# Kernel tuning notes

Measured on AMD Instinct MI355X. Metric: run time of the kernel, lower is better.

The kernel has to match this reference:

```python
import jax, jax.numpy as jnp
import numpy as np

HEADS = 4
DIM_HEAD = 64
DIM = 256
FMAP = 64
SCALE = DIM_HEAD ** -0.5


def setup_inputs() -> dict:
    key = jax.random.key(0)
    k1, k2, k3, k4 = jax.random.split(key, 4)
    inner = HEADS * DIM_HEAD
    fmap = jax.random.normal(k1, (4, DIM, FMAP, FMAP), dtype=jnp.float32)
    # 1x1 conv weight for qkv projection: (3*inner_dim, dim)
    w_qkv = jax.random.normal(k2, (3 * inner, DIM), dtype=jnp.float32) * (DIM ** -0.5)
    # AbsPosEmb parameters, initialized as randn * dim_head**-0.5 (as in BoTNet)
    pos_height = jax.random.normal(k3, (FMAP, DIM_HEAD), dtype=jnp.float32) * SCALE
    pos_width = jax.random.normal(k4, (FMAP, DIM_HEAD), dtype=jnp.float32) * SCALE
    return {"fmap": fmap, "w_qkv": w_qkv, "pos_height": pos_height, "pos_width": pos_width}


def reference(fmap, w_qkv, pos_height, pos_width):
    b, c, h, w = fmap.shape
    hw = h * w
    # 1x1 conv (no bias) == channel matmul
    qkv = jnp.einsum('bchw,oc->bohw', fmap, w_qkv)  # (b, 3*inner, h, w)
    q, k, v = jnp.split(qkv, 3, axis=1)
    # replicate torch .view(b, heads, h*w, -1): raw row-major reshape
    q = q.reshape(b, HEADS, hw, DIM_HEAD) * SCALE
    k = k.reshape(b, HEADS, hw, DIM_HEAD)
    v = v.reshape(b, HEADS, hw, DIM_HEAD)
    sim = jnp.einsum('bhid,bhjd->bhij', q, k)  # (b, heads, hw, hw)
    # absolute positional bias: emb[j] = height[y] + width[x], j = y*w + x
    emb = (pos_height[:, None, :] + pos_width[None, :, :]).reshape(hw, DIM_HEAD)
    sim = sim + jnp.einsum('bhid,jd->bhij', q, emb)
    attn = jax.nn.softmax(sim, axis=-1)
    out = jnp.einsum('bhij,bhjd->bhid', attn, v)  # (b, heads, hw, dim_head)
    # replicate torch .view(b, heads*dim_head, h, w): raw reshape
    return out.reshape(b, HEADS * DIM_HEAD, h, w)
```

## Files before the change

### kernel.cpp

```cpp
#include <hip/hip_runtime.h>


typedef float  f32x4  __attribute__((ext_vector_type(4)));
typedef __bf16 bf16x8 __attribute__((ext_vector_type(8)));
typedef __bf16 bf16x4 __attribute__((ext_vector_type(4)));

__device__ inline float fast_exp2(float x) {
#if __has_builtin(__builtin_amdgcn_exp2f)
  return __builtin_amdgcn_exp2f(x);
#else
  return exp2f(x);
#endif
}

__global__ __launch_bounds__(256) void qkv_proj(
    const float* __restrict__ fmap, const float* __restrict__ w,
    const float* __restrict__ ph,   const float* __restrict__ pw,
    __bf16* __restrict__ Qw, __bf16* __restrict__ Kw, __bf16* __restrict__ Vw)
{
  constexpr int LS = 136;
  __shared__ __bf16 As[64 * LS];
  __shared__ __bf16 Bs[64 * LS];
  const int tid  = threadIdx.x;
  const int wv   = tid >> 6;
  const int lane = tid & 63;
  const int quad = lane >> 4, l15 = lane & 15;
  const int n0 = blockIdx.x * 64;
  const int m0 = blockIdx.y * 64;
  const int b  = blockIdx.z;

  f32x4 sacc[4] = {};

  for (int ks = 0; ks < 2; ++ks) {
    const int kbase = ks * 128;
#pragma unroll
    for (int i = 0; i < 8; ++i) {
      int id = tid + i * 256;
      int r  = id >> 5;
      int c4 = (id & 31) * 4;
      f32x4 v = *(const f32x4*)(w + (size_t)(m0 + r) * 256 + kbase + c4);
      bf16x4 o; o[0]=(__bf16)v[0]; o[1]=(__bf16)v[1]; o[2]=(__bf16)v[2]; o[3]=(__bf16)v[3];
      *(bf16x4*)(&As[r * LS + c4]) = o;
    }
#pragma unroll
    for (int i = 0; i < 2; ++i) {
      int id = tid + i * 256;
      int sg = id & 15;
      int kg = id >> 4;
      const float* base = fmap + ((size_t)b * 256 + kbase + 4 * kg) * 4096 + n0 + 4 * sg;
      f32x4 v0 = *(const f32x4*)(base);
      f32x4 v1 = *(const f32x4*)(base + 4096);
      f32x4 v2 = *(const f32x4*)(base + 8192);
      f32x4 v3 = *(const f32x4*)(base + 12288);
#pragma unroll
      for (int j = 0; j < 4; ++j) {
        bf16x4 o; o[0]=(__bf16)v0[j]; o[1]=(__bf16)v1[j]; o[2]=(__bf16)v2[j]; o[3]=(__bf16)v3[j];
        *(bf16x4*)(&Bs[(4 * sg + j) * LS + 4 * kg]) = o;
      }
    }
    __syncthreads();
#pragma unroll
    for (int k0 = 0; k0 < 128; k0 += 32) {
      bf16x8 af = *(const bf16x8*)(&As[(16 * wv + l15) * LS + k0 + 8 * quad]);
#pragma unroll
      for (int t = 0; t < 4; ++t) {
        bf16x8 bt = *(const bf16x8*)(&Bs[(16 * t + l15) * LS + k0 + 8 * quad]);
        sacc[t] = __builtin_amdgcn_mfma_f32_16x16x32_bf16(af, bt, sacc[t], 0, 0, 0);
      }
    }
    __syncthreads();
  }

  const int region = blockIdx.y >> 2;
  const int obase  = (blockIdx.y & 3) * 64;
#pragma unroll
  for (int t = 0; t < 4; ++t) {
#pragma unroll
    for (int rr = 0; rr < 4; ++rr) {
      int row = 16 * wv + 4 * quad + rr;
      int s   = n0 + 16 * t + l15;
      float val = sacc[t][rr];
      size_t off = ((size_t)(b * 256 + obase + row)) * 4096 + s;
      if (region == 0) {
        Qw[off] = (__bf16)(val * 0.18033688f);
      } else if (region == 1) {
        float bias = ph[row * 64 + (s & 63)] + pw[(s >> 6) * 64 + (s & 63)];
        Kw[off] = (__bf16)(val + bias);
      } else {
        Vw[off] = (__bf16)val;
      }
    }
  }
}

__global__ __launch_bounds__(256) void v_transpose(
    const __bf16* __restrict__ Vw, __bf16* __restrict__ Vt)
{
  __shared__ __bf16 T[64 * 72];
  const int tid = threadIdx.x;
  const int j0  = blockIdx.x * 64;
  const int bh  = blockIdx.y;
  const __bf16* src = Vw + (size_t)bh * 262144;
#pragma unroll
  for (int i = 0; i < 2; ++i) {
    int id = tid + i * 256;
    int r = id >> 3, c = (id & 7) * 8;
    *(bf16x8*)(&T[r * 72 + c]) = *(const bf16x8*)(src + (size_t)(j0 + r) * 64 + c);
  }
  __syncthreads();
#pragma unroll
  for (int i = 0; i < 2; ++i) {
    int id = tid + i * 256;
    int d = id >> 3, jc = (id & 7) * 8;
    bf16x8 o;
#pragma unroll
    for (int z = 0; z < 8; ++z) o[z] = T[(jc + z) * 72 + d];
    *(bf16x8*)(Vt + ((size_t)bh * 64 + d) * 4096 + j0 + jc) = o;
  }
}

__global__ __launch_bounds__(256) void flash_attn(
    const __bf16* __restrict__ Qg, const __bf16* __restrict__ Kg,
    const __bf16* __restrict__ Vtg, float* __restrict__ Og)
{
  constexpr int LS = 72;
  __shared__ __bf16 Ks[64 * LS];
  __shared__ __bf16 Vs[64 * LS];
  const int tid  = threadIdx.x;
  const int wv   = tid >> 6;
  const int lane = tid & 63;
  const int quad = lane >> 4, l15 = lane & 15;
  const int bh = blockIdx.y;
  const int i0 = blockIdx.x * 128;
  const int iw = i0 + 32 * wv;
  const __bf16* Qb = Qg  + (size_t)bh * 262144;
  const __bf16* Kb = Kg  + (size_t)bh * 262144;
  const __bf16* Vb = Vtg + (size_t)bh * 262144;
  float*        Ob = Og  + (size_t)bh * 262144;

  bf16x8 qf[2][2];
#pragma unroll
  for (int m = 0; m < 2; ++m)
#pragma unroll
    for (int c = 0; c < 2; ++c)
      qf[m][c] = *(const bf16x8*)(Qb + (size_t)(iw + 16 * m + l15) * 64 + 32 * c + 8 * quad);

  f32x4 acco[2][4] = {};
  float l_part[2] = {0.f, 0.f};

  const int sr = tid >> 3;
  const int sc = (tid & 7) * 8;

  for (int j0 = 0; j0 < 4096; j0 += 64) {
#pragma unroll
    for (int p = 0; p < 2; ++p) {
      int r  = sr + 32 * p;
      int pr = (r & 0x23) | ((r & 0x0C) << 1) | ((r & 0x10) >> 2);
      *(bf16x8*)(&Ks[r * LS + sc]) = *(const bf16x8*)(Kb + (size_t)(j0 + pr) * 64 + sc);
      *(bf16x8*)(&Vs[r * LS + sc]) = *(const bf16x8*)(Vb + (size_t)r * 4096 + j0 + sc);
    }
    __syncthreads();

    f32x4 sacc[2][4] = {};
#pragma unroll
    for (int c = 0; c < 2; ++c) {
#pragma unroll
      for (int t = 0; t < 4; ++t) {
        bf16x8 ak = *(const bf16x8*)(&Ks[(16 * t + l15) * LS + 32 * c + 8 * quad]);
        sacc[0][t] = __builtin_amdgcn_mfma_f32_16x16x32_bf16(ak, qf[0][c], sacc[0][t], 0, 0, 0);
        sacc[1][t] = __builtin_amdgcn_mfma_f32_16x16x32_bf16(ak, qf[1][c], sacc[1][t], 0, 0, 0);
      }
    }

    bf16x8 pf[2][2];
#pragma unroll
    for (int m = 0; m < 2; ++m) {
#pragma unroll
      for (int t = 0; t < 4; ++t) {
#pragma unroll
        for (int r = 0; r < 4; ++r) {
          float pv = fast_exp2(sacc[m][t][r]);
          sacc[m][t][r] = pv;
          l_part[m] += pv;
        }
      }
#pragma unroll
      for (int c = 0; c < 2; ++c) {
        bf16x8 a;
#pragma unroll
        for (int r = 0; r < 4; ++r) {
          a[r]     = (__bf16)sacc[m][2 * c][r];
          a[4 + r] = (__bf16)sacc[m][2 * c + 1][r];
        }
        pf[m][c] = a;
      }
    }

#pragma unroll
    for (int c = 0; c < 2; ++c) {
#pragma unroll
      for (int t = 0; t < 4; ++t) {
        bf16x8 bv = *(const bf16x8*)(&Vs[(16 * t + l15) * LS + 32 * c + 8 * quad]);
        acco[0][t] = __builtin_amdgcn_mfma_f32_16x16x32_bf16(pf[0][c], bv, acco[0][t], 0, 0, 0);
        acco[1][t] = __builtin_amdgcn_mfma_f32_16x16x32_bf16(pf[1][c], bv, acco[1][t], 0, 0, 0);
      }
    }
    __syncthreads();
  }

  float rl[2][4];
#pragma unroll
  for (int m = 0; m < 2; ++m) {
    float l = l_part[m];
    l += __shfl_xor(l, 16, 64);
    l += __shfl_xor(l, 32, 64);
    float linv = 1.0f / l;
#pragma unroll
    for (int r = 0; r < 4; ++r) rl[m][r] = __shfl(linv, 4 * quad + r, 64);
  }
#pragma unroll
  for (int m = 0; m < 2; ++m)
#pragma unroll
    for (int t = 0; t < 4; ++t)
#pragma unroll
      for (int r = 0; r < 4; ++r)
        Ob[(size_t)(iw + 16 * m + 4 * quad + r) * 64 + 16 * t + l15] =
            acco[m][t][r] * rl[m][r];
}

extern "C" void kernel_launch(void* const* d_in, const int* in_sizes, int n_in,
                              void* d_out, int out_size, void* d_ws, size_t ws_size,
                              hipStream_t stream) {
  const float* fmap = (const float*)d_in[0];
  const float* w    = (const float*)d_in[1];
  const float* ph   = (const float*)d_in[2];
  const float* pw   = (const float*)d_in[3];
  float* out = (float*)d_out;

  __bf16* Qw = (__bf16*)d_ws;
  __bf16* Kw = Qw + 4194304;
  __bf16* Vw = Kw + 4194304;
  __bf16* Vt = Vw + 4194304;

  qkv_proj  <<<dim3(64, 12, 4), 256, 0, stream>>>(fmap, w, ph, pw, Qw, Kw, Vw);
  v_transpose<<<dim3(64, 16),   256, 0, stream>>>(Vw, Vt);
  flash_attn<<<dim3(32, 16),    256, 0, stream>>>(Qw, Kw, Vt, out);
}
```

Baseline: 198.4 us.

## Prefetch K/V tiles via registers, widen attention KV tile and QKV M tile

The attention kernel now processes 128 keys per iteration instead of 64 and keeps the next tile's K and V in registers, loading them from global memory while the current tile is computed. This halves the number of barriers and hides global load latency behind the MFMA work. The row-sum accumulator is split into four partial sums to shorten the dependency chain. The QKV projection computes a 128-row output tile per block, reusing each fmap tile across twice as many rows, in exchange for higher register and LDS use per block that may lower occupancy.

```diff
diff --git a/kernel.cpp b/kernel.cpp
--- a/kernel.cpp
+++ b/kernel.cpp
@@ -19,22 +19,22 @@
     __bf16* __restrict__ Qw, __bf16* __restrict__ Kw, __bf16* __restrict__ Vw)
 {
   constexpr int LS = 136;
-  __shared__ __bf16 As[64 * LS];
+  __shared__ __bf16 As[128 * LS];
   __shared__ __bf16 Bs[64 * LS];
   const int tid  = threadIdx.x;
   const int wv   = tid >> 6;
   const int lane = tid & 63;
   const int quad = lane >> 4, l15 = lane & 15;
   const int n0 = blockIdx.x * 64;
-  const int m0 = blockIdx.y * 64;
+  const int m0 = blockIdx.y * 128;
   const int b  = blockIdx.z;
 
-  f32x4 sacc[4] = {};
+  f32x4 acc[2][4] = {};
 
   for (int ks = 0; ks < 2; ++ks) {
     const int kbase = ks * 128;
 #pragma unroll
-    for (int i = 0; i < 8; ++i) {
+    for (int i = 0; i < 16; ++i) {
       int id = tid + i * 256;
       int r  = id >> 5;
       int c4 = (id & 31) * 4;
@@ -61,33 +61,39 @@
     __syncthreads();
 #pragma unroll
     for (int k0 = 0; k0 < 128; k0 += 32) {
-      bf16x8 af = *(const bf16x8*)(&As[(16 * wv + l15) * LS + k0 + 8 * quad]);
+      bf16x8 af0 = *(const bf16x8*)(&As[(32 * wv      + l15) * LS + k0 + 8 * quad]);
+      bf16x8 af1 = *(const bf16x8*)(&As[(32 * wv + 16 + l15) * LS + k0 + 8 * quad]);
 #pragma unroll
       for (int t = 0; t < 4; ++t) {
         bf16x8 bt = *(const bf16x8*)(&Bs[(16 * t + l15) * LS + k0 + 8 * quad]);
-        sacc[t] = __builtin_amdgcn_mfma_f32_16x16x32_bf16(af, bt, sacc[t], 0, 0, 0);
-      }
-    }
-    __syncthreads();
-  }
-
-  const int region = blockIdx.y >> 2;
-  const int obase  = (blockIdx.y & 3) * 64;
-#pragma unroll
-  for (int t = 0; t < 4; ++t) {
-#pragma unroll
-    for (int rr = 0; rr < 4; ++rr) {
-      int row = 16 * wv + 4 * quad + rr;
-      int s   = n0 + 16 * t + l15;
-      float val = sacc[t][rr];
-      size_t off = ((size_t)(b * 256 + obase + row)) * 4096 + s;
-      if (region == 0) {
-        Qw[off] = (__bf16)(val * 0.18033688f);
-      } else if (region == 1) {
-        float bias = ph[row * 64 + (s & 63)] + pw[(s >> 6) * 64 + (s & 63)];
-        Kw[off] = (__bf16)(val + bias);
-      } else {
-        Vw[off] = (__bf16)val;
+        acc[0][t] = __builtin_amdgcn_mfma_f32_16x16x32_bf16(af0, bt, acc[0][t], 0, 0, 0);
+        acc[1][t] = __builtin_amdgcn_mfma_f32_16x16x32_bf16(af1, bt, acc[1][t], 0, 0, 0);
+      }
+    }
+    __syncthreads();
+  }
+
+  const int region = blockIdx.y >> 1;
+  const int obase  = (blockIdx.y & 1) * 128;
+#pragma unroll
+  for (int mm = 0; mm < 2; ++mm) {
+#pragma unroll
+    for (int t = 0; t < 4; ++t) {
+#pragma unroll
+      for (int rr = 0; rr < 4; ++rr) {
+        int oo = obase + 32 * wv + 16 * mm + 4 * quad + rr;
+        int s  = n0 + 16 * t + l15;
+        float val = acc[mm][t][rr];
+        size_t off = ((size_t)(b * 256 + oo)) * 4096 + s;
+        if (region == 0) {
+          Qw[off] = (__bf16)(val * 0.18033688f);
+        } else if (region == 1) {
+          int g = oo & 63;
+          float bias = ph[g * 64 + (s & 63)] + pw[(s >> 6) * 64 + (s & 63)];
+          Kw[off] = (__bf16)(val + bias);
+        } else {
+          Vw[off] = (__bf16)val;
+        }
       }
     }
   }
@@ -123,16 +129,16 @@
     const __bf16* __restrict__ Qg, const __bf16* __restrict__ Kg,
     const __bf16* __restrict__ Vtg, float* __restrict__ Og)
 {
-  constexpr int LS = 72;
-  __shared__ __bf16 Ks[64 * LS];
-  __shared__ __bf16 Vs[64 * LS];
+  constexpr int LSK = 72;
+  constexpr int LSV = 136;
+  __shared__ __bf16 Ks[128 * LSK];
+  __shared__ __bf16 Vs[64 * LSV];
   const int tid  = threadIdx.x;
   const int wv   = tid >> 6;
   const int lane = tid & 63;
   const int quad = lane >> 4, l15 = lane & 15;
   const int bh = blockIdx.y;
-  const int i0 = blockIdx.x * 128;
-  const int iw = i0 + 32 * wv;
+  const int iw = blockIdx.x * 128 + 32 * wv;
   const __bf16* Qb = Qg  + (size_t)bh * 262144;
   const __bf16* Kb = Kg  + (size_t)bh * 262144;
   const __bf16* Vb = Vtg + (size_t)bh * 262144;
@@ -145,64 +151,90 @@
     for (int c = 0; c < 2; ++c)
       qf[m][c] = *(const bf16x8*)(Qb + (size_t)(iw + 16 * m + l15) * 64 + 32 * c + 8 * quad);
 
+  const int krow = tid >> 3;
+  const int ksc  = (tid & 7) * 8;
+  const int vrow = tid >> 4;
+  const int vjc  = (tid & 15) * 8;
+  const __bf16* kptr[4]; int kdst[4];
+  const __bf16* vptr[4]; int vdst[4];
+#pragma unroll
+  for (int p = 0; p < 4; ++p) {
+    int r  = krow + 32 * p;
+    int pr = (r & 0x63) | ((r & 0x0C) << 1) | ((r & 0x10) >> 2);
+    kptr[p] = Kb + (size_t)pr * 64 + ksc;
+    kdst[p] = r * LSK + ksc;
+    int d  = vrow + 16 * p;
+    vptr[p] = Vb + (size_t)d * 4096 + vjc;
+    vdst[p] = d * LSV + vjc;
+  }
+
+  bf16x8 kreg[4], vreg[4];
+#pragma unroll
+  for (int p = 0; p < 4; ++p) {
+    kreg[p] = *(const bf16x8*)kptr[p]; kptr[p] += 8192;
+    vreg[p] = *(const bf16x8*)vptr[p]; vptr[p] += 128;
+  }
+
   f32x4 acco[2][4] = {};
-  float l_part[2] = {0.f, 0.f};
-
-  const int sr = tid >> 3;
-  const int sc = (tid & 7) * 8;
-
-  for (int j0 = 0; j0 < 4096; j0 += 64) {
-#pragma unroll
-    for (int p = 0; p < 2; ++p) {
-      int r  = sr + 32 * p;
-      int pr = (r & 0x23) | ((r & 0x0C) << 1) | ((r & 0x10) >> 2);
-      *(bf16x8*)(&Ks[r * LS + sc]) = *(const bf16x8*)(Kb + (size_t)(j0 + pr) * 64 + sc);
-      *(bf16x8*)(&Vs[r * LS + sc]) = *(const bf16x8*)(Vb + (size_t)r * 4096 + j0 + sc);
-    }
-    __syncthreads();
-
-    f32x4 sacc[2][4] = {};
+  f32x4 l4[2] = {};
+
+  for (int it = 0; it < 32; ++it) {
+#pragma unroll
+    for (int p = 0; p < 4; ++p) {
+      *(bf16x8*)(&Ks[kdst[p]]) = kreg[p];
+      *(bf16x8*)(&Vs[vdst[p]]) = vreg[p];
+    }
+    __syncthreads();
+    if (it < 31) {
+#pragma unroll
+      for (int p = 0; p < 4; ++p) {
+        kreg[p] = *(const bf16x8*)kptr[p]; kptr[p] += 8192;
+        vreg[p] = *(const bf16x8*)vptr[p]; vptr[p] += 128;
+      }
+    }
+
+    f32x4 sacc[2][8] = {};
 #pragma unroll
     for (int c = 0; c < 2; ++c) {
 #pragma unroll
-      for (int t = 0; t < 4; ++t) {
-        bf16x8 ak = *(const bf16x8*)(&Ks[(16 * t + l15) * LS + 32 * c + 8 * quad]);
+      for (int t = 0; t < 8; ++t) {
+        bf16x8 ak = *(const bf16x8*)(&Ks[(16 * t + l15) * LSK + 32 * c + 8 * quad]);
         sacc[0][t] = __builtin_amdgcn_mfma_f32_16x16x32_bf16(ak, qf[0][c], sacc[0][t], 0, 0, 0);
         sacc[1][t] = __builtin_amdgcn_mfma_f32_16x16x32_bf16(ak, qf[1][c], sacc[1][t], 0, 0, 0);
       }
     }
 
-    bf16x8 pf[2][2];
+    bf16x8 pf[2][4];
 #pragma unroll
     for (int m = 0; m < 2; ++m) {
 #pragma unroll
-      for (int t = 0; t < 4; ++t) {
+      for (int t = 0; t < 8; ++t) {
 #pragma unroll
         for (int r = 0; r < 4; ++r) {
           float pv = fast_exp2(sacc[m][t][r]);
           sacc[m][t][r] = pv;
-          l_part[m] += pv;
+          l4[m][r] += pv;
         }
       }
 #pragma unroll
-      for (int c = 0; c < 2; ++c) {
+      for (int c2 = 0; c2 < 4; ++c2) {
         bf16x8 a;
 #pragma unroll
         for (int r = 0; r < 4; ++r) {
-          a[r]     = (__bf16)sacc[m][2 * c][r];
-          a[4 + r] = (__bf16)sacc[m][2 * c + 1][r];
+          a[r]     = (__bf16)sacc[m][2 * c2][r];
+          a[4 + r] = (__bf16)sacc[m][2 * c2 + 1][r];
         }
-        pf[m][c] = a;
-      }
-    }
-
-#pragma unroll
-    for (int c = 0; c < 2; ++c) {
+        pf[m][c2] = a;
+      }
+    }
+
+#pragma unroll
+    for (int c2 = 0; c2 < 4; ++c2) {
 #pragma unroll
       for (int t = 0; t < 4; ++t) {
-        bf16x8 bv = *(const bf16x8*)(&Vs[(16 * t + l15) * LS + 32 * c + 8 * quad]);
-        acco[0][t] = __builtin_amdgcn_mfma_f32_16x16x32_bf16(pf[0][c], bv, acco[0][t], 0, 0, 0);
-        acco[1][t] = __builtin_amdgcn_mfma_f32_16x16x32_bf16(pf[1][c], bv, acco[1][t], 0, 0, 0);
+        bf16x8 bv = *(const bf16x8*)(&Vs[(16 * t + l15) * LSV + 32 * c2 + 8 * quad]);
+        acco[0][t] = __builtin_amdgcn_mfma_f32_16x16x32_bf16(pf[0][c2], bv, acco[0][t], 0, 0, 0);
+        acco[1][t] = __builtin_amdgcn_mfma_f32_16x16x32_bf16(pf[1][c2], bv, acco[1][t], 0, 0, 0);
       }
     }
     __syncthreads();
@@ -211,7 +243,7 @@
   float rl[2][4];
 #pragma unroll
   for (int m = 0; m < 2; ++m) {
-    float l = l_part[m];
+    float l = (l4[m][0] + l4[m][1]) + (l4[m][2] + l4[m][3]);
     l += __shfl_xor(l, 16, 64);
     l += __shfl_xor(l, 32, 64);
     float linv = 1.0f / l;
@@ -242,7 +274,7 @@
   __bf16* Vw = Kw + 4194304;
   __bf16* Vt = Vw + 4194304;
 
-  qkv_proj  <<<dim3(64, 12, 4), 256, 0, stream>>>(fmap, w, ph, pw, Qw, Kw, Vw);
-  v_transpose<<<dim3(64, 16),   256, 0, stream>>>(Vw, Vt);
-  flash_attn<<<dim3(32, 16),    256, 0, stream>>>(Qw, Kw, Vt, out);
-}
+  qkv_proj  <<<dim3(64, 6, 4), 256, 0, stream>>>(fmap, w, ph, pw, Qw, Kw, Vw);
+  v_transpose<<<dim3(64, 16),  256, 0, stream>>>(Vw, Vt);
+  flash_attn<<<dim3(32, 16),   256, 0, stream>>>(Qw, Kw, Vt, out);
+}
```

After: 223.9 us. 12.8% more time.

## Split attention KV range across two blocks and combine partials

Applied to the files above, without the earlier changes.

Splits the key/value sequence into two halves via a z grid dimension, doubling the block count from 512 to 1024 to fill more compute units, then adds a combine kernel that sums the partial outputs and row sums and normalizes. Shared memory tiles switch from padded rows to XOR-swizzled unpadded rows, and occupancy is hinted with launch bounds. The first partial is stored in bf16 in the freed Vw buffer, adding a precision loss, an extra kernel launch and extra global traffic.

```diff
diff --git a/kernel.cpp b/kernel.cpp
--- a/kernel.cpp
+++ b/kernel.cpp
@@ -119,24 +119,24 @@
   }
 }
 
-__global__ __launch_bounds__(256) void flash_attn(
+__global__ __launch_bounds__(256, 4) void flash_attn(
     const __bf16* __restrict__ Qg, const __bf16* __restrict__ Kg,
-    const __bf16* __restrict__ Vtg, float* __restrict__ Og)
-{
-  constexpr int LS = 72;
-  __shared__ __bf16 Ks[64 * LS];
-  __shared__ __bf16 Vs[64 * LS];
+    const __bf16* __restrict__ Vtg, __bf16* __restrict__ OP0,
+    float* __restrict__ lws, float* __restrict__ Og)
+{
+  __shared__ __bf16 Ks[64 * 64];
+  __shared__ __bf16 Vs[64 * 64];
   const int tid  = threadIdx.x;
   const int wv   = tid >> 6;
   const int lane = tid & 63;
   const int quad = lane >> 4, l15 = lane & 15;
   const int bh = blockIdx.y;
-  const int i0 = blockIdx.x * 128;
-  const int iw = i0 + 32 * wv;
+  const int z  = blockIdx.z;
+  const int iw = blockIdx.x * 128 + 32 * wv;
+  const int jbase = z * 2048;
   const __bf16* Qb = Qg  + (size_t)bh * 262144;
   const __bf16* Kb = Kg  + (size_t)bh * 262144;
   const __bf16* Vb = Vtg + (size_t)bh * 262144;
-  float*        Ob = Og  + (size_t)bh * 262144;
 
   bf16x8 qf[2][2];
 #pragma unroll
@@ -145,20 +145,32 @@
     for (int c = 0; c < 2; ++c)
       qf[m][c] = *(const bf16x8*)(Qb + (size_t)(iw + 16 * m + l15) * 64 + 32 * c + 8 * quad);
 
+  const int kr  = tid >> 3;
+  const int kch = tid & 7;
+  const int r0 = kr,      r1 = kr + 32;
+  const int pr0 = (r0 & 0x23) | ((r0 & 0x0C) << 1) | ((r0 & 0x10) >> 2);
+  const int pr1 = (r1 & 0x23) | ((r1 & 0x0C) << 1) | ((r1 & 0x10) >> 2);
+  const int dst0 = r0 * 64 + ((kch ^ (r0 & 7)) * 8);
+  const int dst1 = r1 * 64 + ((kch ^ (r1 & 7)) * 8);
+  const __bf16* kp0 = Kb + (size_t)(jbase + pr0) * 64 + kch * 8;
+  const __bf16* kp1 = Kb + (size_t)(jbase + pr1) * 64 + kch * 8;
+  const __bf16* vp0 = Vb + (size_t)r0 * 4096 + jbase + kch * 8;
+  const __bf16* vp1 = Vb + (size_t)r1 * 4096 + jbase + kch * 8;
+
   f32x4 acco[2][4] = {};
-  float l_part[2] = {0.f, 0.f};
-
-  const int sr = tid >> 3;
-  const int sc = (tid & 7) * 8;
-
-  for (int j0 = 0; j0 < 4096; j0 += 64) {
-#pragma unroll
-    for (int p = 0; p < 2; ++p) {
-      int r  = sr + 32 * p;
-      int pr = (r & 0x23) | ((r & 0x0C) << 1) | ((r & 0x10) >> 2);
-      *(bf16x8*)(&Ks[r * LS + sc]) = *(const bf16x8*)(Kb + (size_t)(j0 + pr) * 64 + sc);
-      *(bf16x8*)(&Vs[r * LS + sc]) = *(const bf16x8*)(Vb + (size_t)r * 4096 + j0 + sc);
-    }
+  f32x4 l4[2] = {};
+
+  const int swz = (l15 & 7);
+
+  for (int it = 0; it < 32; ++it) {
+    bf16x8 k0 = *(const bf16x8*)kp0; kp0 += 4096;
+    bf16x8 k1 = *(const bf16x8*)kp1; kp1 += 4096;
+    bf16x8 v0 = *(const bf16x8*)vp0; vp0 += 64;
+    bf16x8 v1 = *(const bf16x8*)vp1; vp1 += 64;
+    *(bf16x8*)(&Ks[dst0]) = k0;
+    *(bf16x8*)(&Ks[dst1]) = k1;
+    *(bf16x8*)(&Vs[dst0]) = v0;
+    *(bf16x8*)(&Vs[dst1]) = v1;
     __syncthreads();
 
     f32x4 sacc[2][4] = {};
@@ -166,7 +178,7 @@
     for (int c = 0; c < 2; ++c) {
 #pragma unroll
       for (int t = 0; t < 4; ++t) {
-        bf16x8 ak = *(const bf16x8*)(&Ks[(16 * t + l15) * LS + 32 * c + 8 * quad]);
+        bf16x8 ak = *(const bf16x8*)(&Ks[(16 * t + l15) * 64 + (((4 * c + quad) ^ swz) * 8)]);
         sacc[0][t] = __builtin_amdgcn_mfma_f32_16x16x32_bf16(ak, qf[0][c], sacc[0][t], 0, 0, 0);
         sacc[1][t] = __builtin_amdgcn_mfma_f32_16x16x32_bf16(ak, qf[1][c], sacc[1][t], 0, 0, 0);
       }
@@ -181,51 +193,77 @@
         for (int r = 0; r < 4; ++r) {
           float pv = fast_exp2(sacc[m][t][r]);
           sacc[m][t][r] = pv;
-          l_part[m] += pv;
+          l4[m][r] += pv;
         }
       }
 #pragma unroll
-      for (int c = 0; c < 2; ++c) {
+      for (int c2 = 0; c2 < 2; ++c2) {
         bf16x8 a;
 #pragma unroll
         for (int r = 0; r < 4; ++r) {
-          a[r]     = (__bf16)sacc[m][2 * c][r];
-          a[4 + r] = (__bf16)sacc[m][2 * c + 1][r];
+          a[r]     = (__bf16)sacc[m][2 * c2][r];
+          a[4 + r] = (__bf16)sacc[m][2 * c2 + 1][r];
         }
-        pf[m][c] = a;
-      }
-    }
-
-#pragma unroll
-    for (int c = 0; c < 2; ++c) {
-#pragma unroll
-      for (int t = 0; t < 4; ++t) {
-        bf16x8 bv = *(const bf16x8*)(&Vs[(16 * t + l15) * LS + 32 * c + 8 * quad]);
-        acco[0][t] = __builtin_amdgcn_mfma_f32_16x16x32_bf16(pf[0][c], bv, acco[0][t], 0, 0, 0);
-        acco[1][t] = __builtin_amdgcn_mfma_f32_16x16x32_bf16(pf[1][c], bv, acco[1][t], 0, 0, 0);
-      }
-    }
-    __syncthreads();
-  }
-
-  float rl[2][4];
+        pf[m][c2] = a;
+      }
+    }
+
+#pragma unroll
+    for (int c2 = 0; c2 < 2; ++c2) {
+#pragma unroll
+      for (int t = 0; t < 4; ++t) {
+        bf16x8 bv = *(const bf16x8*)(&Vs[(16 * t + l15) * 64 + (((4 * c2 + quad) ^ swz) * 8)]);
+        acco[0][t] = __builtin_amdgcn_mfma_f32_16x16x32_bf16(pf[0][c2], bv, acco[0][t], 0, 0, 0);
+        acco[1][t] = __builtin_amdgcn_mfma_f32_16x16x32_bf16(pf[1][c2], bv, acco[1][t], 0, 0, 0);
+      }
+    }
+    __syncthreads();
+  }
+
 #pragma unroll
   for (int m = 0; m < 2; ++m) {
-    float l = l_part[m];
+    float l = (l4[m][0] + l4[m][1]) + (l4[m][2] + l4[m][3]);
     l += __shfl_xor(l, 16, 64);
     l += __shfl_xor(l, 32, 64);
-    float linv = 1.0f / l;
-#pragma unroll
-    for (int r = 0; r < 4; ++r) rl[m][r] = __shfl(linv, 4 * quad + r, 64);
-  }
-#pragma unroll
-  for (int m = 0; m < 2; ++m)
-#pragma unroll
-    for (int t = 0; t < 4; ++t)
-#pragma unroll
-      for (int r = 0; r < 4; ++r)
-        Ob[(size_t)(iw + 16 * m + 4 * quad + r) * 64 + 16 * t + l15] =
-            acco[m][t][r] * rl[m][r];
+    if (quad == 0)
+      lws[z * 65536 + bh * 4096 + iw + 16 * m + l15] = l;
+  }
+  if (z == 0) {
+    __bf16* Ob = OP0 + (size_t)bh * 262144;
+#pragma unroll
+    for (int m = 0; m < 2; ++m)
+#pragma unroll
+      for (int t = 0; t < 4; ++t)
+#pragma unroll
+        for (int r = 0; r < 4; ++r)
+          Ob[(size_t)(iw + 16 * m + 4 * quad + r) * 64 + 16 * t + l15] =
+              (__bf16)acco[m][t][r];
+  } else {
+    float* Ob = Og + (size_t)bh * 262144;
+#pragma unroll
+    for (int m = 0; m < 2; ++m)
+#pragma unroll
+      for (int t = 0; t < 4; ++t)
+#pragma unroll
+        for (int r = 0; r < 4; ++r)
+          Ob[(size_t)(iw + 16 * m + 4 * quad + r) * 64 + 16 * t + l15] =
+              acco[m][t][r];
+  }
+}
+
+__global__ __launch_bounds__(256) void combine(
+    const __bf16* __restrict__ OP0, const float* __restrict__ lws,
+    float* __restrict__ Og)
+{
+  int idx = blockIdx.x * 256 + threadIdx.x;
+  int row = idx >> 4;
+  float inv = 1.0f / (lws[row] + lws[65536 + row]);
+  f32x4 o = ((const f32x4*)Og)[idx];
+  bf16x4 p = ((const bf16x4*)OP0)[idx];
+  f32x4 r;
+#pragma unroll
+  for (int k = 0; k < 4; ++k) r[k] = (o[k] + (float)p[k]) * inv;
+  ((f32x4*)Og)[idx] = r;
 }
 
 extern "C" void kernel_launch(void* const* d_in, const int* in_sizes, int n_in,
@@ -241,8 +279,10 @@
   __bf16* Kw = Qw + 4194304;
   __bf16* Vw = Kw + 4194304;
   __bf16* Vt = Vw + 4194304;
-
-  qkv_proj  <<<dim3(64, 12, 4), 256, 0, stream>>>(fmap, w, ph, pw, Qw, Kw, Vw);
-  v_transpose<<<dim3(64, 16),   256, 0, stream>>>(Vw, Vt);
-  flash_attn<<<dim3(32, 16),    256, 0, stream>>>(Qw, Kw, Vt, out);
-}
+  float*  lws = (float*)(Vt + 4194304);
+
+  qkv_proj   <<<dim3(64, 12, 4), 256, 0, stream>>>(fmap, w, ph, pw, Qw, Kw, Vw);
+  v_transpose<<<dim3(64, 16),    256, 0, stream>>>(Vw, Vt);
+  flash_attn <<<dim3(32, 16, 2), 256, 0, stream>>>(Qw, Kw, Vt, Vw , lws, out);
+  combine    <<<dim3(4096),      256, 0, stream>>>(Vw , lws, out);
+}
```

Result: faster. 188.1 us (-5.2%).
